# Optimization experiments

Measured on AMD Instinct MI355X. Metric: run time of the kernel, lower is better.

Reference implementation:

```python
import jax, jax.numpy as jnp
import numpy as np

LOSS_CUTOFF = 100000.0
EPS = 1e-08

B, S, A = 512, 512, 200


def setup_inputs() -> dict:
    key = jax.random.key(0)
    k1, k2, k3, k4 = jax.random.split(key, 4)
    logits = jax.random.normal(k1, (B, S, A), dtype=jnp.float32)
    actions = jax.random.randint(k2, (B, S), 0, A, dtype=jnp.int64)
    rewards = jax.random.uniform(k3, (B, S), dtype=jnp.float32)
    terminals = jax.random.uniform(k4, (B, S), dtype=jnp.float32)
    return {"logits": logits, "actions": actions, "rewards": rewards, "terminals": terminals}


def reference(logits, actions, rewards, terminals):
    # log_p: [B, S, A], masked by (1 - terminals)
    log_p = jax.nn.log_softmax(logits, axis=2) * (1.0 - terminals)[:, :, None]
    # gather per-timestep action log-prob: [B, S] -> total_logp: [B]
    action_logp = jnp.take_along_axis(log_p, actions[:, :, None], axis=2)[..., 0]
    total_logp = -jnp.sum(action_logp, axis=1)  # [B]
    total_rewards = jnp.sum(rewards, axis=1)    # [B]
    # 'mean' branch: masked mean over total_logp < loss_cutoff
    prod = total_logp * total_rewards
    mask = total_logp < LOSS_CUTOFF
    cnt = jnp.sum(mask.astype(prod.dtype))
    rewardloss_mean = jnp.sum(jnp.where(mask, prod, 0.0)) / cnt
    mean_loss = rewardloss_mean / (jnp.mean(jnp.abs(total_rewards)) + EPS)
    return mean_loss
```

## Files before the change

### kernel.cpp

```cpp
#include <hip/hip_runtime.h>
#include <hip/hip_bf16.h>
#include <math.h>


#define BDIM 512
#define SDIM 512
#define ADIM 200
#define ROWS_PER_WAVE 8
#define WAVES_PER_BLOCK 4
#define ROWS_PER_BLOCK (ROWS_PER_WAVE * WAVES_PER_BLOCK)

__global__ __launch_bounds__(256) void pg_row_kernel(
    const float* __restrict__ logits,
    const int*   __restrict__ actions,
    const float* __restrict__ rewards,
    const float* __restrict__ terminals,
    float* __restrict__ ws_logp,
    float* __restrict__ ws_rew)
{
    const int lane = threadIdx.x & 63;
    const int wave = threadIdx.x >> 6;
    const int row0 = blockIdx.x * ROWS_PER_BLOCK + wave * ROWS_PER_WAVE;

    const int  cl  = (lane < 50) ? lane : 49;
    const bool act = (lane < 50);

    float4 v[ROWS_PER_WAVE];
    #pragma unroll
    for (int i = 0; i < ROWS_PER_WAVE; ++i) {
        const float4* rowp = (const float4*)(logits + (size_t)(row0 + i) * ADIM);
        v[i] = rowp[cl];
    }

    float e[ROWS_PER_WAVE];
    #pragma unroll
    for (int i = 0; i < ROWS_PER_WAVE; ++i) {
        const float s = __expf(v[i].x) + __expf(v[i].y) +
                        __expf(v[i].z) + __expf(v[i].w);
        e[i] = act ? s : 0.0f;
    }

    #pragma unroll
    for (int off = 32; off >= 1; off >>= 1) {
        #pragma unroll
        for (int i = 0; i < ROWS_PER_WAVE; ++i)
            e[i] += __shfl_down(e[i], off);
    }

    float acc_logp = 0.0f, acc_rew = 0.0f;
    #pragma unroll
    for (int i = 0; i < ROWS_PER_WAVE; ++i) {
        const int   row = row0 + i;
        const float lse = __logf(e[i]);
        const float xa  = logits[(size_t)row * ADIM + actions[row]];
        acc_logp += (xa - lse) * (1.0f - terminals[row]);
        acc_rew  += rewards[row];
    }

    __shared__ float s_logp[WAVES_PER_BLOCK], s_rew[WAVES_PER_BLOCK];
    if (lane == 0) { s_logp[wave] = acc_logp; s_rew[wave] = acc_rew; }
    __syncthreads();
    if (threadIdx.x == 0) {
        float tl = 0.0f, tr = 0.0f;
        #pragma unroll
        for (int w = 0; w < WAVES_PER_BLOCK; ++w) { tl += s_logp[w]; tr += s_rew[w]; }
        const int b = (blockIdx.x * ROWS_PER_BLOCK) >> 9;
        atomicAdd(&ws_logp[b], tl);
        atomicAdd(&ws_rew[b],  tr);
    }
}

__global__ __launch_bounds__(512) void pg_final_kernel(
    const float* __restrict__ ws_logp,
    const float* __restrict__ ws_rew,
    float* __restrict__ out)
{
    const int tid  = threadIdx.x;
    const int lane = tid & 63;
    const int wave = tid >> 6;

    const float total_logp = -ws_logp[tid];
    const float total_rew  =  ws_rew[tid];

    float mp   = (total_logp < 100000.0f) ? total_logp * total_rew : 0.0f;
    float cnt  = (total_logp < 100000.0f) ? 1.0f : 0.0f;
    float arew = fabsf(total_rew);

    #pragma unroll
    for (int off = 32; off >= 1; off >>= 1) {
        mp   += __shfl_down(mp,   off);
        cnt  += __shfl_down(cnt,  off);
        arew += __shfl_down(arew, off);
    }

    __shared__ float s_mp[8], s_cnt[8], s_ab[8];
    if (lane == 0) { s_mp[wave] = mp; s_cnt[wave] = cnt; s_ab[wave] = arew; }
    __syncthreads();
    if (tid == 0) {
        float smp = 0.0f, scnt = 0.0f, sab = 0.0f;
        #pragma unroll
        for (int i = 0; i < 8; ++i) { smp += s_mp[i]; scnt += s_cnt[i]; sab += s_ab[i]; }
        const float rewardloss_mean = smp / scnt;
        out[0] = rewardloss_mean / (sab / (float)BDIM + 1e-8f);
    }
}

extern "C" void kernel_launch(void* const* d_in, const int* in_sizes, int n_in,
                              void* d_out, int out_size, void* d_ws, size_t ws_size,
                              hipStream_t stream) {
    const float* logits    = (const float*)d_in[0];
    const int*   actions   = (const int*)  d_in[1];
    const float* rewards   = (const float*)d_in[2];
    const float* terminals = (const float*)d_in[3];

    float* ws_logp = (float*)d_ws;
    float* ws_rew  = ws_logp + BDIM;

    hipMemsetAsync(d_ws, 0, 2 * BDIM * sizeof(float), stream);

    pg_row_kernel<<<(BDIM * SDIM) / ROWS_PER_BLOCK, 256, 0, stream>>>(
        logits, actions, rewards, terminals, ws_logp, ws_rew);

    pg_final_kernel<<<1, 512, 0, stream>>>(ws_logp, ws_rew, (float*)d_out);
}
```

Before: 288.4 us.

## Loop four row groups per block, use DPP wave reduction, hoist scalar loads

Each block now handles four iterations of 32 rows, which cuts the grid to a quarter and reduces the number of per-block atomics and LDS reductions. The shuffle-based wave sum is replaced by a DPP row/broadcast reduction followed by a readlane of lane 63. Action indices are loaded first so the gathered action logit, terminal and reward loads are issued before the exp work. Launch bounds now request 4 blocks per CU. The risk is fewer waves in flight to hide memory latency on a kernel that is bandwidth-bound (about 210 MB of logits).

```diff
diff --git a/kernel.cpp b/kernel.cpp
--- a/kernel.cpp
+++ b/kernel.cpp
@@ -8,9 +8,23 @@
 #define ADIM 200
 #define ROWS_PER_WAVE 8
 #define WAVES_PER_BLOCK 4
-#define ROWS_PER_BLOCK (ROWS_PER_WAVE * WAVES_PER_BLOCK)
+#define ROWS_PER_ITER (ROWS_PER_WAVE * WAVES_PER_BLOCK)
+#define ITERS 4
+#define ROWS_PER_BLOCK (ROWS_PER_ITER * ITERS)
+#define NBLOCKS ((BDIM * SDIM) / ROWS_PER_BLOCK)
 
-__global__ __launch_bounds__(256) void pg_row_kernel(
+__device__ __forceinline__ float dpp_reduce_add(float x) {
+    int t;
+    t = __builtin_amdgcn_update_dpp(0, __float_as_int(x), 0x111, 0xf, 0xf, true); x += __int_as_float(t);
+    t = __builtin_amdgcn_update_dpp(0, __float_as_int(x), 0x112, 0xf, 0xf, true); x += __int_as_float(t);
+    t = __builtin_amdgcn_update_dpp(0, __float_as_int(x), 0x114, 0xf, 0xf, true); x += __int_as_float(t);
+    t = __builtin_amdgcn_update_dpp(0, __float_as_int(x), 0x118, 0xf, 0xf, true); x += __int_as_float(t);
+    t = __builtin_amdgcn_update_dpp(0, __float_as_int(x), 0x142, 0xa, 0xf, true); x += __int_as_float(t);
+    t = __builtin_amdgcn_update_dpp(0, __float_as_int(x), 0x143, 0xc, 0xf, true); x += __int_as_float(t);
+    return x;
+}
+
+__global__ __launch_bounds__(256, 4) void pg_row_kernel(
     const float* __restrict__ logits,
     const int*   __restrict__ actions,
     const float* __restrict__ rewards,
@@ -20,41 +34,44 @@
 {
     const int lane = threadIdx.x & 63;
     const int wave = threadIdx.x >> 6;
-    const int row0 = blockIdx.x * ROWS_PER_BLOCK + wave * ROWS_PER_WAVE;
+    const int block_row0 = blockIdx.x * ROWS_PER_BLOCK;
+    const int b = block_row0 >> 9;
 
-    const int  cl  = (lane < 50) ? lane : 49;
-    const bool act = (lane < 50);
+    const int  cl = (lane < 50) ? lane : 49;
 
-    float4 v[ROWS_PER_WAVE];
-    #pragma unroll
-    for (int i = 0; i < ROWS_PER_WAVE; ++i) {
-        const float4* rowp = (const float4*)(logits + (size_t)(row0 + i) * ADIM);
-        v[i] = rowp[cl];
-    }
+    float acc_logp = 0.0f, acc_rew = 0.0f;
 
-    float e[ROWS_PER_WAVE];
-    #pragma unroll
-    for (int i = 0; i < ROWS_PER_WAVE; ++i) {
-        const float s = __expf(v[i].x) + __expf(v[i].y) +
-                        __expf(v[i].z) + __expf(v[i].w);
-        e[i] = act ? s : 0.0f;
-    }
+    for (int it = 0; it < ITERS; ++it) {
+        const int row0 = block_row0 + it * ROWS_PER_ITER + wave * ROWS_PER_WAVE;
 
-    #pragma unroll
-    for (int off = 32; off >= 1; off >>= 1) {
+        int a[ROWS_PER_WAVE];
+        #pragma unroll
+        for (int i = 0; i < ROWS_PER_WAVE; ++i) a[i] = actions[row0 + i];
+
+        float4 v[ROWS_PER_WAVE];
         #pragma unroll
         for (int i = 0; i < ROWS_PER_WAVE; ++i)
-            e[i] += __shfl_down(e[i], off);
-    }
+            v[i] = ((const float4*)(logits + (size_t)(row0 + i) * ADIM))[cl];
 
-    float acc_logp = 0.0f, acc_rew = 0.0f;
-    #pragma unroll
-    for (int i = 0; i < ROWS_PER_WAVE; ++i) {
-        const int   row = row0 + i;
-        const float lse = __logf(e[i]);
-        const float xa  = logits[(size_t)row * ADIM + actions[row]];
-        acc_logp += (xa - lse) * (1.0f - terminals[row]);
-        acc_rew  += rewards[row];
+        float xa[ROWS_PER_WAVE], tm[ROWS_PER_WAVE], rw[ROWS_PER_WAVE];
+        #pragma unroll
+        for (int i = 0; i < ROWS_PER_WAVE; ++i) {
+            xa[i] = logits[(size_t)(row0 + i) * ADIM + a[i]];
+            tm[i] = terminals[row0 + i];
+            rw[i] = rewards[row0 + i];
+        }
+
+        #pragma unroll
+        for (int i = 0; i < ROWS_PER_WAVE; ++i) {
+            float s = __expf(v[i].x) + __expf(v[i].y) +
+                      __expf(v[i].z) + __expf(v[i].w);
+            s = (lane < 50) ? s : 0.0f;
+            const float tot  = dpp_reduce_add(s);
+            const float etot = __int_as_float(
+                __builtin_amdgcn_readlane(__float_as_int(tot), 63));
+            acc_logp += (xa[i] - __logf(etot)) * (1.0f - tm[i]);
+            acc_rew  += rw[i];
+        }
     }
 
     __shared__ float s_logp[WAVES_PER_BLOCK], s_rew[WAVES_PER_BLOCK];
@@ -64,7 +81,6 @@
         float tl = 0.0f, tr = 0.0f;
         #pragma unroll
         for (int w = 0; w < WAVES_PER_BLOCK; ++w) { tl += s_logp[w]; tr += s_rew[w]; }
-        const int b = (blockIdx.x * ROWS_PER_BLOCK) >> 9;
         atomicAdd(&ws_logp[b], tl);
         atomicAdd(&ws_rew[b],  tr);
     }
@@ -118,7 +134,7 @@
 
     hipMemsetAsync(d_ws, 0, 2 * BDIM * sizeof(float), stream);
 
-    pg_row_kernel<<<(BDIM * SDIM) / ROWS_PER_BLOCK, 256, 0, stream>>>(
+    pg_row_kernel<<<NBLOCKS, 256, 0, stream>>>(
         logits, actions, rewards, terminals, ws_logp, ws_rew);
 
     pg_final_kernel<<<1, 512, 0, stream>>>(ws_logp, ws_rew, (float*)d_out);
```

Result: no change. 292.1 us (+1.3%).
